# Optimization experiments

Measured on AMD Instinct MI355X. Metric: run time of the kernel, lower is better.

The kernel has to match this reference:

```python
import jax, jax.numpy as jnp
import numpy as np

N = 8192  # number of observations (rows of configuration)
D = 128   # embedding dimension


def _pair_indices(n):
    """Pair ordering of the original TF loop: for upper in 2..n-1, lower in 0..upper-1.
    (Pair (0,1) is never emitted by the original code.)"""
    counts = np.arange(2, n, dtype=np.int64)          # block u contributes u pairs
    uppers = np.repeat(counts, counts)
    starts = np.concatenate([np.zeros(1, np.int64), np.cumsum(counts)[:-1]])
    lowers = np.arange(uppers.shape[0], dtype=np.int64) - np.repeat(starts, counts)
    return lowers.astype(np.int32), uppers.astype(np.int32)


def setup_inputs() -> dict:
    key = jax.random.key(0)
    inputs = jax.random.normal(key, (N, D), dtype=jnp.float32)
    return {"inputs": inputs}


def reference(inputs):
    n = inputs.shape[0]
    lowers, uppers = _pair_indices(n)  # static (numpy) index arrays
    # trace(X^T (e_l-e_u)(e_l-e_u)^T X) == ||x_l - x_u||^2
    # Gram trick: ||x_l - x_u||^2 = ||x_l||^2 + ||x_u||^2 - 2 <x_l, x_u>
    sq = jnp.sum(inputs * inputs, axis=1)          # [n]
    gram = inputs @ inputs.T                        # [n, n]
    dists = sq[lowers] + sq[uppers] - 2.0 * gram[lowers, uppers]
    # Original TensorArray has size (n^2-n)/2 but only (n^2-n)/2 - 1 slots are
    # written (pair (0,1) is skipped); the last slot stacks as zero.
    out = jnp.concatenate([dists, jnp.zeros((1,), dists.dtype)])
    return out[None, :]  # tf.expand_dims(..., 0)
```

## Files before the change

### kernel.cpp

```cpp
#include <hip/hip_runtime.h>
#include <hip/hip_bf16.h>

#define NROWS 8192
#define DIM   128
#define NT    64
#define NBLK  (NT * (NT + 1) / 2)
#define TOTAL_OUT 33550336u

typedef short bf16x8 __attribute__((ext_vector_type(8)));
typedef float f32x4  __attribute__((ext_vector_type(4)));
typedef unsigned short u16x8 __attribute__((ext_vector_type(8)));

static __device__ inline unsigned short f32_to_bf16(float f) {
    unsigned int u = __float_as_uint(f);
    u += 0x7FFFu + ((u >> 16) & 1u);
    return (unsigned short)(u >> 16);
}

__global__ __launch_bounds__(256) void prep_kernel(const float* __restrict__ X,
                                                   unsigned short* __restrict__ Xr,
                                                   float* __restrict__ sq,
                                                   float* __restrict__ out) {
    __shared__ float sm[16][17];
    const int g = blockIdx.x;
    const int t = threadIdx.x;
    const int kk = t >> 6, lane = t & 63;
    const int lrow = lane & 15, kgrp = lane >> 4;

    const float* src = X + (size_t)(g * 16 + lrow) * DIM + (kk * 4 + kgrp) * 8;
    const float4 v0 = *reinterpret_cast<const float4*>(src);
    const float4 v1 = *reinterpret_cast<const float4*>(src + 4);

    u16x8 h;
    h[0] = f32_to_bf16(v0.x); h[1] = f32_to_bf16(v0.y);
    h[2] = f32_to_bf16(v0.z); h[3] = f32_to_bf16(v0.w);
    h[4] = f32_to_bf16(v1.x); h[5] = f32_to_bf16(v1.y);
    h[6] = f32_to_bf16(v1.z); h[7] = f32_to_bf16(v1.w);
    *reinterpret_cast<u16x8*>(Xr + ((size_t)(g * 4 + kk) * 64 + lane) * 8) = h;

    float p = v0.x * v0.x + v0.y * v0.y + v0.z * v0.z + v0.w * v0.w
            + v1.x * v1.x + v1.y * v1.y + v1.z * v1.z + v1.w * v1.w;
    sm[lrow][kk * 4 + kgrp] = p;
    __syncthreads();
    if (t < 16) {
        float s = 0.f;
        #pragma unroll
        for (int j = 0; j < 16; ++j) s += sm[t][j];
        sq[g * 16 + t] = s;
    }
    if (g == 0 && t == 0) out[TOTAL_OUT - 1] = 0.0f;
}

__global__ __launch_bounds__(256, 4) void pdist_kernel(const unsigned short* __restrict__ Xr,
                                                       const float* __restrict__ sq,
                                                       float* __restrict__ out) {
    const int t  = threadIdx.x;
    const int bt = blockIdx.x;
    int bj = (int)((sqrtf(8.0f * (float)bt + 1.0f) - 1.0f) * 0.5f);
    while ((bj + 1) * (bj + 2) / 2 <= bt) ++bj;
    while (bj * (bj + 1) / 2 > bt) --bj;
    const int bi = bt - bj * (bj + 1) / 2;

    const int wid  = t >> 6;
    const int lane = t & 63;
    const int wr   = wid >> 1;
    const int wc   = wid & 1;
    const int lrow = lane & 15;
    const int kgrp = lane >> 4;

    const bf16x8* __restrict__ F = reinterpret_cast<const bf16x8*>(Xr);
    const int gA = bi * 8 + wr * 4;
    const int gB = bj * 8 + wc * 4;

    f32x4 acc[4][4];
    const f32x4 fzero = {0.f, 0.f, 0.f, 0.f};
    #pragma unroll
    for (int m = 0; m < 4; ++m)
        #pragma unroll
        for (int n = 0; n < 4; ++n) acc[m][n] = fzero;

    bf16x8 a[2][4], b[2][4];
    #pragma unroll
    for (int m = 0; m < 4; ++m) {
        a[0][m] = F[((gA + m) * 4 + 0) * 64 + lane];
        b[0][m] = F[((gB + m) * 4 + 0) * 64 + lane];
    }
    #pragma unroll
    for (int kk = 0; kk < 4; ++kk) {
        const int cur = kk & 1, nxt = cur ^ 1;
        if (kk < 3) {
            #pragma unroll
            for (int m = 0; m < 4; ++m) {
                a[nxt][m] = F[((gA + m) * 4 + kk + 1) * 64 + lane];
                b[nxt][m] = F[((gB + m) * 4 + kk + 1) * 64 + lane];
            }
        }
        #pragma unroll
        for (int m = 0; m < 4; ++m)
            #pragma unroll
            for (int n = 0; n < 4; ++n)
                acc[m][n] = __builtin_amdgcn_mfma_f32_16x16x32_bf16(a[cur][m], b[cur][n], acc[m][n], 0, 0, 0);
    }

    const int l0 = bi * 128 + wr * 64;
    const int u0 = bj * 128 + wc * 64;
    const int rj = kgrp * 4;

    float squ[4];
    f32x4 sql[4];
    #pragma unroll
    for (int n = 0; n < 4; ++n) squ[n] = sq[u0 + n * 16 + lrow];
    #pragma unroll
    for (int m = 0; m < 4; ++m)
        sql[m] = *reinterpret_cast<const f32x4*>(sq + l0 + m * 16 + rj);

    if (bi != bj) {
        #pragma unroll
        for (int m = 0; m < 4; ++m) {
            #pragma unroll
            for (int n = 0; n < 4; ++n) {
                const int u = u0 + n * 16 + lrow;
                const size_t base = ((size_t)u * (u - 1)) / 2 - 1 + (size_t)(l0 + m * 16 + rj);
                f32x4 d;
                #pragma unroll
                for (int j = 0; j < 4; ++j) d[j] = sql[m][j] + squ[n] - 2.0f * acc[m][n][j];
                __builtin_memcpy(out + base, &d, 16);
            }
        }
    } else {
        #pragma unroll
        for (int m = 0; m < 4; ++m) {
            #pragma unroll
            for (int n = 0; n < 4; ++n) {
                const int u = u0 + n * 16 + lrow;
                #pragma unroll
                for (int j = 0; j < 4; ++j) {
                    const int l = l0 + m * 16 + rj + j;
                    if (l < u && u >= 2) {
                        out[((size_t)u * (u - 1)) / 2 - 1 + l] = sql[m][j] + squ[n] - 2.0f * acc[m][n][j];
                    }
                }
            }
        }
    }
}

extern "C" void kernel_launch(void* const* d_in, const int* in_sizes, int n_in,
                              void* d_out, int out_size, void* d_ws, size_t ws_size,
                              hipStream_t stream) {
    const float* X = (const float*)d_in[0];
    float* out = (float*)d_out;
    unsigned short* Xr = (unsigned short*)d_ws;
    float* sq = (float*)((char*)d_ws + (size_t)NROWS * DIM * 2);

    prep_kernel<<<NROWS / 16, 256, 0, stream>>>(X, Xr, sq, out);
    pdist_kernel<<<NBLK, 256, 0, stream>>>(Xr, sq, out);
}
```

Baseline: 54.08 us.

## Persistent column-strip blocks iterating over row tiles with register-resident B

Replaces the one-block-per-128x128-triangle-tile grid with 1088 blocks, each owning a 64-column strip and looping over a chunk of up to four 128-row tiles. The B fragments stay in registers across iterations while A is double-buffered, which is meant to cut redundant global fragment loads and block launch overhead. Blocks run in reverse order so the larger strips are scheduled first. Launch bounds drop to 2 blocks per CU to make room for the larger register footprint, which lowers occupancy for what is mostly a store-bound kernel.

```diff
diff --git a/kernel.cpp b/kernel.cpp
--- a/kernel.cpp
+++ b/kernel.cpp
@@ -3,9 +3,9 @@
 
 #define NROWS 8192
 #define DIM   128
-#define NT    64
-#define NBLK  (NT * (NT + 1) / 2)
 #define TOTAL_OUT 33550336u
+#define CHUNK 4
+#define NBLK_P 1088
 
 typedef short bf16x8 __attribute__((ext_vector_type(8)));
 typedef float f32x4  __attribute__((ext_vector_type(4)));
@@ -16,6 +16,9 @@
     u += 0x7FFFu + ((u >> 16) & 1u);
     return (unsigned short)(u >> 16);
 }
+
+static __device__ inline int S4(int a) { int q = a >> 2, r = a & 3; return 2 * q * (q + 1) + r * (q + 1); }
+static __device__ inline int cumf(int uj) { int a = uj >> 1, b = uj & 1; return 2 * S4(a) + b * ((a >> 2) + 1); }
 
 __global__ __launch_bounds__(256) void prep_kernel(const float* __restrict__ X,
                                                    unsigned short* __restrict__ Xr,
@@ -51,15 +54,18 @@
     if (g == 0 && t == 0) out[TOTAL_OUT - 1] = 0.0f;
 }
 
-__global__ __launch_bounds__(256, 4) void pdist_kernel(const unsigned short* __restrict__ Xr,
+__global__ __launch_bounds__(256, 2) void pdist_kernel(const unsigned short* __restrict__ Xr,
                                                        const float* __restrict__ sq,
                                                        float* __restrict__ out) {
-    const int t  = threadIdx.x;
-    const int bt = blockIdx.x;
-    int bj = (int)((sqrtf(8.0f * (float)bt + 1.0f) - 1.0f) * 0.5f);
-    while ((bj + 1) * (bj + 2) / 2 <= bt) ++bj;
-    while (bj * (bj + 1) / 2 > bt) --bj;
-    const int bi = bt - bj * (bj + 1) / 2;
+    const int t   = threadIdx.x;
+    const int rid = NBLK_P - 1 - (int)blockIdx.x;
+    int lo = 0, hi = 127;
+    while (lo < hi) { int mid = (lo + hi + 1) >> 1; if (cumf(mid) <= rid) lo = mid; else hi = mid - 1; }
+    const int uj    = lo;
+    const int chunk = rid - cumf(uj);
+    const int ext   = (uj >> 1) + 1;
+    const int t0    = chunk * CHUNK;
+    const int t1    = (t0 + CHUNK < ext) ? (t0 + CHUNK) : ext;
 
     const int wid  = t >> 6;
     const int lane = t & 63;
@@ -69,75 +75,88 @@
     const int kgrp = lane >> 4;
 
     const bf16x8* __restrict__ F = reinterpret_cast<const bf16x8*>(Xr);
-    const int gA = bi * 8 + wr * 4;
-    const int gB = bj * 8 + wc * 4;
 
-    f32x4 acc[4][4];
-    const f32x4 fzero = {0.f, 0.f, 0.f, 0.f};
+    bf16x8 b[2][4];
     #pragma unroll
-    for (int m = 0; m < 4; ++m)
+    for (int n = 0; n < 2; ++n)
         #pragma unroll
-        for (int n = 0; n < 4; ++n) acc[m][n] = fzero;
+        for (int kk = 0; kk < 4; ++kk)
+            b[n][kk] = F[(((uj * 4 + wc * 2 + n) * 4) + kk) * 64 + lane];
 
-    bf16x8 a[2][4], b[2][4];
+    const int u0 = uj * 64 + wc * 32;
+    float squ[2];
     #pragma unroll
-    for (int m = 0; m < 4; ++m) {
-        a[0][m] = F[((gA + m) * 4 + 0) * 64 + lane];
-        b[0][m] = F[((gB + m) * 4 + 0) * 64 + lane];
-    }
-    #pragma unroll
-    for (int kk = 0; kk < 4; ++kk) {
-        const int cur = kk & 1, nxt = cur ^ 1;
-        if (kk < 3) {
-            #pragma unroll
-            for (int m = 0; m < 4; ++m) {
-                a[nxt][m] = F[((gA + m) * 4 + kk + 1) * 64 + lane];
-                b[nxt][m] = F[((gB + m) * 4 + kk + 1) * 64 + lane];
-            }
-        }
+    for (int n = 0; n < 2; ++n) squ[n] = sq[u0 + n * 16 + lrow];
+
+    bf16x8 aA[4][4], aB[4][4];
+    auto loadA = [&](bf16x8 (&buf)[4][4], int lt) {
         #pragma unroll
         for (int m = 0; m < 4; ++m)
             #pragma unroll
-            for (int n = 0; n < 4; ++n)
-                acc[m][n] = __builtin_amdgcn_mfma_f32_16x16x32_bf16(a[cur][m], b[cur][n], acc[m][n], 0, 0, 0);
-    }
+            for (int kk = 0; kk < 4; ++kk)
+                buf[m][kk] = F[((lt * 8 + wr * 4 + m) * 4 + kk) * 64 + lane];
+    };
 
-    const int l0 = bi * 128 + wr * 64;
-    const int u0 = bj * 128 + wc * 64;
-    const int rj = kgrp * 4;
+    loadA(aA, t0);
+    for (int lt = t0; lt < t1; ++lt) {
+        f32x4 acc[4][2];
+        #pragma unroll
+        for (int m = 0; m < 4; ++m) { acc[m][0] = (f32x4){0.f,0.f,0.f,0.f}; acc[m][1] = (f32x4){0.f,0.f,0.f,0.f}; }
 
-    float squ[4];
-    f32x4 sql[4];
-    #pragma unroll
-    for (int n = 0; n < 4; ++n) squ[n] = sq[u0 + n * 16 + lrow];
-    #pragma unroll
-    for (int m = 0; m < 4; ++m)
-        sql[m] = *reinterpret_cast<const f32x4*>(sq + l0 + m * 16 + rj);
+        if (((lt - t0) & 1) == 0) {
+            if (lt + 1 < t1) loadA(aB, lt + 1);
+            #pragma unroll
+            for (int kk = 0; kk < 4; ++kk)
+                #pragma unroll
+                for (int m = 0; m < 4; ++m) {
+                    acc[m][0] = __builtin_amdgcn_mfma_f32_16x16x32_bf16(aA[m][kk], b[0][kk], acc[m][0], 0, 0, 0);
+                    acc[m][1] = __builtin_amdgcn_mfma_f32_16x16x32_bf16(aA[m][kk], b[1][kk], acc[m][1], 0, 0, 0);
+                }
+        } else {
+            if (lt + 1 < t1) loadA(aA, lt + 1);
+            #pragma unroll
+            for (int kk = 0; kk < 4; ++kk)
+                #pragma unroll
+                for (int m = 0; m < 4; ++m) {
+                    acc[m][0] = __builtin_amdgcn_mfma_f32_16x16x32_bf16(aB[m][kk], b[0][kk], acc[m][0], 0, 0, 0);
+                    acc[m][1] = __builtin_amdgcn_mfma_f32_16x16x32_bf16(aB[m][kk], b[1][kk], acc[m][1], 0, 0, 0);
+                }
+        }
 
-    if (bi != bj) {
+        const int lbase = lt * 128 + wr * 64;
+        f32x4 sql[4];
         #pragma unroll
-        for (int m = 0; m < 4; ++m) {
+        for (int m = 0; m < 4; ++m)
+            sql[m] = *reinterpret_cast<const f32x4*>(sq + lbase + m * 16 + kgrp * 4);
+
+        if (lt * 128 + 128 <= uj * 64) {
             #pragma unroll
-            for (int n = 0; n < 4; ++n) {
-                const int u = u0 + n * 16 + lrow;
-                const size_t base = ((size_t)u * (u - 1)) / 2 - 1 + (size_t)(l0 + m * 16 + rj);
-                f32x4 d;
+            for (int m = 0; m < 4; ++m) {
                 #pragma unroll
-                for (int j = 0; j < 4; ++j) d[j] = sql[m][j] + squ[n] - 2.0f * acc[m][n][j];
-                __builtin_memcpy(out + base, &d, 16);
+                for (int n = 0; n < 2; ++n) {
+                    const int u = u0 + n * 16 + lrow;
+                    const size_t base = (size_t)u * (size_t)(u - 1) / 2 - 1
+                                      + (size_t)(lbase + m * 16 + kgrp * 4);
+                    f32x4 d;
+                    #pragma unroll
+                    for (int j = 0; j < 4; ++j) d[j] = sql[m][j] + squ[n] - 2.0f * acc[m][n][j];
+                    __builtin_memcpy(out + base, &d, 16);
+                }
             }
-        }
-    } else {
-        #pragma unroll
-        for (int m = 0; m < 4; ++m) {
+        } else {
             #pragma unroll
-            for (int n = 0; n < 4; ++n) {
-                const int u = u0 + n * 16 + lrow;
+            for (int m = 0; m < 4; ++m) {
                 #pragma unroll
-                for (int j = 0; j < 4; ++j) {
-                    const int l = l0 + m * 16 + rj + j;
-                    if (l < u && u >= 2) {
-                        out[((size_t)u * (u - 1)) / 2 - 1 + l] = sql[m][j] + squ[n] - 2.0f * acc[m][n][j];
+                for (int n = 0; n < 2; ++n) {
+                    const int u = u0 + n * 16 + lrow;
+                    if (u >= 2) {
+                        #pragma unroll
+                        for (int j = 0; j < 4; ++j) {
+                            const int l = lbase + m * 16 + kgrp * 4 + j;
+                            if (l < u)
+                                out[(size_t)u * (size_t)(u - 1) / 2 - 1 + l] =
+                                    sql[m][j] + squ[n] - 2.0f * acc[m][n][j];
+                        }
                     }
                 }
             }
@@ -154,5 +173,5 @@
     float* sq = (float*)((char*)d_ws + (size_t)NROWS * DIM * 2);
 
     prep_kernel<<<NROWS / 16, 256, 0, stream>>>(X, Xr, sq, out);
-    pdist_kernel<<<NBLK, 256, 0, stream>>>(Xr, sq, out);
+    pdist_kernel<<<NBLK_P, 256, 0, stream>>>(Xr, sq, out);
 }
```

Result: slower. 84.73 us (+56.7%).
